# Performance work log

Measured on AMD Instinct MI355X. Metric: run time of the kernel, lower is better.

Reference implementation:

```python
import jax, jax.numpy as jnp
import numpy as np

D_MODEL = 1024
NUM_HEADS = 16
HEAD_DIM = D_MODEL // NUM_HEADS


def setup_inputs() -> dict:
    key = jax.random.key(0)
    ks = jax.random.split(key, 10)
    B, T, D = 2, 2048, D_MODEL
    scale = 1.0 / np.sqrt(D)
    inp = {
        "x": jax.random.normal(ks[0], (B, T, D), dtype=jnp.float32),
        "mask": jax.random.randint(ks[1], (B, T), 0, 2).astype(jnp.int32),
        "Wq": jax.random.normal(ks[2], (D, D), dtype=jnp.float32) * scale,
        "bq": jnp.zeros((D,), dtype=jnp.float32),
        "Wk": jax.random.normal(ks[3], (D, D), dtype=jnp.float32) * scale,
        "bk": jnp.zeros((D,), dtype=jnp.float32),
        "Wv": jax.random.normal(ks[4], (D, D), dtype=jnp.float32) * scale,
        "bv": jnp.zeros((D,), dtype=jnp.float32),
        "Wo": jax.random.normal(ks[5], (D, D), dtype=jnp.float32) * scale,
        "bo": jnp.zeros((D,), dtype=jnp.float32),
    }
    return inp


def reference(x, mask, Wq, bq, Wk, bk, Wv, bv, Wo, bo):
    B, T, D = x.shape
    H, Hd = NUM_HEADS, HEAD_DIM
    # torch Linear: y = x @ W.T + b
    Q = (x @ Wq.T + bq).reshape(B, T, H, Hd).transpose(0, 2, 1, 3)  # [B,H,T,Hd]
    K = (x @ Wk.T + bk).reshape(B, T, H, Hd).transpose(0, 2, 1, 3)
    V = (x @ Wv.T + bv).reshape(B, T, H, Hd).transpose(0, 2, 1, 3)
    scores = jnp.einsum("bhqd,bhkd->bhqk", Q, K) / jnp.sqrt(jnp.float32(Hd))
    # key padding mask: 1=valid, 0=pad -> -inf on padded keys
    key_pad = (mask == 0)[:, None, None, :]  # [B,1,1,T]
    scores = jnp.where(key_pad, -jnp.inf, scores)
    attn = jax.nn.softmax(scores, axis=-1)  # [B,H,T,T]
    # dropout p=0.0 (inference): identity
    context = jnp.einsum("bhqk,bhkd->bhqd", attn, V)  # [B,H,T,Hd]
    context = context.transpose(0, 2, 1, 3).reshape(B, T, D)
    output = context @ Wo.T + bo
    return (output, attn)
```

## Files before the change

kernel.cpp:

```cpp
#include <hip/hip_runtime.h>
#include <math.h>

#define SEQ   2048
#define BATCH 2
#define DM    1024
#define NH    16
#define HD    64
#define MTOT  (BATCH*SEQ)
#define NQSZ  ((size_t)BATCH*NH*SEQ*HD)

typedef __bf16 bf16_t;
typedef __bf16 bf16x4 __attribute__((ext_vector_type(4)));
typedef __bf16 bf16x8 __attribute__((ext_vector_type(8)));
typedef float  f32x4  __attribute__((ext_vector_type(4)));

typedef __attribute__((address_space(1))) void glob_void;
typedef __attribute__((address_space(3))) void lds_void;
#define GL2LDS(gp, lp) __builtin_amdgcn_global_load_lds( \
    (glob_void*)(gp), (lds_void*)(lp), 16, 0, 0)

__global__ __launch_bounds__(256)
void cvt_bf16(const float* __restrict__ in, bf16_t* __restrict__ out, int n)
{
    int i = (blockIdx.x * 256 + threadIdx.x) * 4;
    if (i >= n) return;
    float4 f = *(const float4*)(in + i);
    bf16x4 h;
    h.x = (__bf16)f.x; h.y = (__bf16)f.y; h.z = (__bf16)f.z; h.w = (__bf16)f.w;
    *(bf16x4*)(out + i) = h;
}

template<int MODE>
__global__ __launch_bounds__(256)
void gemm_bt(const bf16_t* __restrict__ A, const bf16_t* __restrict__ W,
             const float* __restrict__ b0p, const float* __restrict__ b1p,
             const float* __restrict__ b2p, void* __restrict__ outp)
{
    __shared__ __align__(16) bf16_t As[128 * 32];
    __shared__ __align__(16) bf16_t Bs[128 * 32];
    const int n0 = blockIdx.x * 128, m0 = blockIdx.y * 128;
    const int tid = threadIdx.x, lane = tid & 63, wave = tid >> 6;
    const int wm = (wave >> 1) * 64, wn = (wave & 1) * 64;
    const int srow = wave * 32 + (lane >> 2);
    const int scol = (lane & 3) * 8;
    const int fr = lane & 15, fk = (lane >> 4) * 8;
    const bf16_t* gA = &A[(size_t)(m0 + srow) * DM + scol];
    const bf16_t* gB = &W[(size_t)(n0 + srow) * DM + scol];
    bf16_t* lA = &As[wave * 1024];
    bf16_t* lB = &Bs[wave * 1024];
    f32x4 acc[4][4] = {};
    for (int k0 = 0; k0 < DM; k0 += 32) {
        GL2LDS(gA,            lA);
        GL2LDS(gA + 16 * DM,  lA + 16 * 32);
        GL2LDS(gB,            lB);
        GL2LDS(gB + 16 * DM,  lB + 16 * 32);
        gA += 32; gB += 32;
        __syncthreads();
        bf16x8 af[4], bv[4];
        #pragma unroll
        for (int mi = 0; mi < 4; ++mi)
            af[mi] = *(const bf16x8*)&As[(wm + mi * 16 + fr) * 32 + fk];
        #pragma unroll
        for (int ni = 0; ni < 4; ++ni)
            bv[ni] = *(const bf16x8*)&Bs[(wn + ni * 16 + fr) * 32 + fk];
        #pragma unroll
        for (int mi = 0; mi < 4; ++mi)
            #pragma unroll
            for (int ni = 0; ni < 4; ++ni)
                acc[mi][ni] = __builtin_amdgcn_mfma_f32_16x16x32_bf16(af[mi], bv[ni], acc[mi][ni], 0, 0, 0);
        __syncthreads();
    }
    const int cr = (lane >> 4) * 4, cc = lane & 15;
    #pragma unroll
    for (int mi = 0; mi < 4; ++mi) {
        #pragma unroll
        for (int ni = 0; ni < 4; ++ni) {
            const int n = n0 + wn + ni * 16 + cc;
            float bn;
            if (MODE == 0) {
                const int which = n >> 10, nn = n & 1023;
                const float* bp = which == 0 ? b0p : (which == 1 ? b1p : b2p);
                bn = bp[nn];
            } else {
                bn = b0p[n];
            }
            #pragma unroll
            for (int v = 0; v < 4; ++v) {
                const int m = m0 + wm + mi * 16 + cr + v;
                const float val = acc[mi][ni][v] + bn;
                if (MODE == 0) {
                    const int which = n >> 10, nn = n & 1023;
                    const int b_ = m >> 11, t = m & (SEQ - 1);
                    const int h = nn >> 6, hd = nn & 63;
                    ((bf16_t*)outp)[(size_t)which * NQSZ +
                        (((size_t)(b_ * NH + h)) * SEQ + t) * HD + hd] = (__bf16)val;
                } else {
                    ((float*)outp)[(size_t)m * DM + n] = val;
                }
            }
        }
    }
}

__global__ __launch_bounds__(256)
void transpose_v(const bf16_t* __restrict__ Vb, bf16_t* __restrict__ Vt)
{
    const int bh = blockIdx.y, t0 = blockIdx.x * 64;
    __shared__ bf16_t L[64][72];
    const bf16_t* src = Vb + (size_t)bh * SEQ * HD;
    bf16_t* dst = Vt + (size_t)bh * HD * SEQ;
    for (int i = threadIdx.x; i < 64 * 64; i += 256) {
        int r = i >> 6, c = i & 63;
        L[c][r] = src[(size_t)(t0 + r) * HD + c];
    }
    __syncthreads();
    for (int i = threadIdx.x; i < 64 * 64; i += 256) {
        int hd = i >> 6, c = i & 63;
        dst[(size_t)hd * SEQ + t0 + c] = L[hd][c];
    }
}

__global__ __launch_bounds__(256, 2)
void fused_attn(const bf16_t* __restrict__ Q, const bf16_t* __restrict__ K,
                const bf16_t* __restrict__ Vt, const int* __restrict__ mask,
                float* __restrict__ attn, bf16_t* __restrict__ ctxb)
{
    __shared__ __align__(16) bf16_t Qs[2 * 128 * 32];
    __shared__ __align__(16) bf16_t Ks[2 * 128 * 32];
    __shared__ __align__(16) bf16_t Vs[4 * 64 * 32];
    __shared__ __align__(16) bf16_t Ps[4][4 * 32 * 32];

    const int bid = blockIdx.x;
    const int grp = bid & 7, g2 = bid >> 3;
    const int bh = grp * 4 + (g2 >> 4);
    const int qt = g2 & 15;
    const int b = bh >> 4, h = bh & 15;
    const int q0 = qt * 128;

    const bf16_t* Qb  = Q  + (size_t)bh * SEQ * HD;
    const bf16_t* Kb  = K  + (size_t)bh * SEQ * HD;
    const bf16_t* Vtb = Vt + (size_t)bh * HD * SEQ;
    const int*    mb  = mask + b * SEQ;
    float*        Ab  = attn + (size_t)bh * SEQ * SEQ;

    const int tid = threadIdx.x, lane = tid & 63, wave = tid >> 6;
    const int wm = wave * 32;
    const int fr = lane & 15, fg = lane >> 4, fk = fg * 8;
    const int cr = fg * 4, cc = fr;
    const int rsw = ((fr >> 2) & 3) << 3;
    const int wsw = fg << 3;

    {
        const int r = tid >> 2, kq = (tid & 3) * 16;
        #pragma unroll
        for (int rr = 0; rr < 2; ++rr)
            #pragma unroll
            for (int j = 0; j < 2; ++j) {
                const int k = kq + j * 8;
                *(uint4*)&Qs[(k >> 5) * 4096 + (r + rr * 64) * 32 + (k & 31)] =
                    *(const uint4*)&Qb[(size_t)(q0 + r + rr * 64) * HD + k];
            }
    }
    __syncthreads();
    bf16x8 qf[2][2];
    #pragma unroll
    for (int mi = 0; mi < 2; ++mi)
        #pragma unroll
        for (int c = 0; c < 2; ++c)
            qf[mi][c] = *(const bf16x8*)&Qs[c * 4096 + (wm + mi * 16 + fr) * 32 + fk];

    float rm[2][4], rl[2][4];
    #pragma unroll
    for (int mi = 0; mi < 2; ++mi)
        #pragma unroll
        for (int v = 0; v < 4; ++v) { rm[mi][v] = -1e30f; rl[mi][v] = 0.f; }

    for (int kt0 = 0; kt0 < SEQ; kt0 += 128) {
        __syncthreads();
        {
            const int r = tid >> 2, kq = (tid & 3) * 16;
            #pragma unroll
            for (int rr = 0; rr < 2; ++rr)
                #pragma unroll
                for (int j = 0; j < 2; ++j) {
                    const int k = kq + j * 8;
                    *(uint4*)&Ks[(k >> 5) * 4096 + (r + rr * 64) * 32 + (k & 31)] =
                        *(const uint4*)&Kb[(size_t)(kt0 + r + rr * 64) * HD + k];
                }
        }
        __syncthreads();
        float ma[8];
        #pragma unroll
        for (int ni = 0; ni < 8; ++ni)
            ma[ni] = mb[kt0 + ni * 16 + cc] ? 0.f : -1e30f;
        f32x4 acc[2][8] = {};
        #pragma unroll
        for (int ni = 0; ni < 8; ++ni) {
            bf16x8 b0 = *(const bf16x8*)&Ks[(ni * 16 + fr) * 32 + fk];
            bf16x8 b1 = *(const bf16x8*)&Ks[4096 + (ni * 16 + fr) * 32 + fk];
            acc[0][ni] = __builtin_amdgcn_mfma_f32_16x16x32_bf16(qf[0][0], b0, acc[0][ni], 0, 0, 0);
            acc[1][ni] = __builtin_amdgcn_mfma_f32_16x16x32_bf16(qf[1][0], b0, acc[1][ni], 0, 0, 0);
            acc[0][ni] = __builtin_amdgcn_mfma_f32_16x16x32_bf16(qf[0][1], b1, acc[0][ni], 0, 0, 0);
            acc[1][ni] = __builtin_amdgcn_mfma_f32_16x16x32_bf16(qf[1][1], b1, acc[1][ni], 0, 0, 0);
        }
        #pragma unroll
        for (int mi = 0; mi < 2; ++mi) {
            #pragma unroll
            for (int v = 0; v < 4; ++v) {
                float tm = -1e30f;
                #pragma unroll
                for (int ni = 0; ni < 8; ++ni) {
                    float s = acc[mi][ni][v] * 0.125f + ma[ni];
                    acc[mi][ni][v] = s;
                    tm = fmaxf(tm, s);
                }
                tm = fmaxf(tm, __shfl_xor(tm, 1));
                tm = fmaxf(tm, __shfl_xor(tm, 2));
                tm = fmaxf(tm, __shfl_xor(tm, 4));
                tm = fmaxf(tm, __shfl_xor(tm, 8));
                const float mn = fmaxf(rm[mi][v], tm);
                float ls = 0.f;
                #pragma unroll
                for (int ni = 0; ni < 8; ++ni)
                    ls += __expf(acc[mi][ni][v] - mn);
                ls += __shfl_xor(ls, 1);
                ls += __shfl_xor(ls, 2);
                ls += __shfl_xor(ls, 4);
                ls += __shfl_xor(ls, 8);
                rl[mi][v] = rl[mi][v] * __expf(rm[mi][v] - mn) + ls;
                rm[mi][v] = mn;
            }
        }
    }

    float invl[2][4];
    #pragma unroll
    for (int mi = 0; mi < 2; ++mi)
        #pragma unroll
        for (int v = 0; v < 4; ++v)
            invl[mi][v] = 1.0f / rl[mi][v];

    f32x4 oac[2][4] = {};
    bf16_t* Pw = &Ps[wave][0];
    for (int kt0 = 0; kt0 < SEQ; kt0 += 128) {
        __syncthreads();
        {
            const int r = tid >> 2, kq = (tid & 3) * 16;
            #pragma unroll
            for (int rr = 0; rr < 2; ++rr)
                #pragma unroll
                for (int j = 0; j < 2; ++j) {
                    const int k = kq + j * 8;
                    *(uint4*)&Ks[(k >> 5) * 4096 + (r + rr * 64) * 32 + (k & 31)] =
                        *(const uint4*)&Kb[(size_t)(kt0 + r + rr * 64) * HD + k];
                }
        }
        {
            const int hd = tid >> 2, ks = tid & 3;
            #pragma unroll
            for (int j = 0; j < 4; ++j)
                *(uint4*)&Vs[ks * 2048 + hd * 32 + j * 8] =
                    *(const uint4*)&Vtb[(size_t)hd * SEQ + kt0 + ks * 32 + j * 8];
        }
        __syncthreads();
        float ma[8];
        #pragma unroll
        for (int ni = 0; ni < 8; ++ni)
            ma[ni] = mb[kt0 + ni * 16 + cc] ? 0.f : -1e30f;
        f32x4 acc[2][8] = {};
        #pragma unroll
        for (int ni = 0; ni < 8; ++ni) {
            bf16x8 b0 = *(const bf16x8*)&Ks[(ni * 16 + fr) * 32 + fk];
            bf16x8 b1 = *(const bf16x8*)&Ks[4096 + (ni * 16 + fr) * 32 + fk];
            acc[0][ni] = __builtin_amdgcn_mfma_f32_16x16x32_bf16(qf[0][0], b0, acc[0][ni], 0, 0, 0);
            acc[1][ni] = __builtin_amdgcn_mfma_f32_16x16x32_bf16(qf[1][0], b0, acc[1][ni], 0, 0, 0);
            acc[0][ni] = __builtin_amdgcn_mfma_f32_16x16x32_bf16(qf[0][1], b1, acc[0][ni], 0, 0, 0);
            acc[1][ni] = __builtin_amdgcn_mfma_f32_16x16x32_bf16(qf[1][1], b1, acc[1][ni], 0, 0, 0);
        }
        #pragma unroll
        for (int mi = 0; mi < 2; ++mi) {
            #pragma unroll
            for (int ni = 0; ni < 8; ++ni) {
                const int ks = ni >> 1, k2 = (ni & 1) * 16 + cc;
                #pragma unroll
                for (int v = 0; v < 4; ++v) {
                    const int rowl = mi * 16 + cr + v;
                    float s = acc[mi][ni][v] * 0.125f + ma[ni];
                    float p = __expf(s - rm[mi][v]) * invl[mi][v];
                    Ab[(size_t)(q0 + wm + rowl) * SEQ + kt0 + ni * 16 + cc] = p;
                    Pw[(ks * 1024 + rowl * 32 + k2) ^ wsw] = (__bf16)p;
                }
            }
        }
        #pragma unroll
        for (int ks = 0; ks < 4; ++ks) {
            bf16x8 pf[2];
            #pragma unroll
            for (int mi = 0; mi < 2; ++mi)
                pf[mi] = *(const bf16x8*)&Pw[(ks * 1024 + (mi * 16 + fr) * 32 + fk) ^ rsw];
            #pragma unroll
            for (int ni = 0; ni < 4; ++ni) {
                bf16x8 vf = *(const bf16x8*)&Vs[ks * 2048 + (ni * 16 + fr) * 32 + fk];
                oac[0][ni] = __builtin_amdgcn_mfma_f32_16x16x32_bf16(pf[0], vf, oac[0][ni], 0, 0, 0);
                oac[1][ni] = __builtin_amdgcn_mfma_f32_16x16x32_bf16(pf[1], vf, oac[1][ni], 0, 0, 0);
            }
        }
    }
    #pragma unroll
    for (int mi = 0; mi < 2; ++mi) {
        #pragma unroll
        for (int ni = 0; ni < 4; ++ni) {
            #pragma unroll
            for (int v = 0; v < 4; ++v) {
                const int t = q0 + wm + mi * 16 + cr + v;
                ctxb[((size_t)b * SEQ + t) * DM + h * HD + ni * 16 + cc] = (__bf16)oac[mi][ni][v];
            }
        }
    }
}

extern "C" void kernel_launch(void* const* d_in, const int* in_sizes, int n_in,
                              void* d_out, int out_size, void* d_ws, size_t ws_size,
                              hipStream_t stream)
{
    const float* x   = (const float*)d_in[0];
    const int*  mask = (const int*)d_in[1];
    const float* Wq  = (const float*)d_in[2];
    const float* bq  = (const float*)d_in[3];
    const float* Wk  = (const float*)d_in[4];
    const float* bk  = (const float*)d_in[5];
    const float* Wv  = (const float*)d_in[6];
    const float* bv  = (const float*)d_in[7];
    const float* Wo  = (const float*)d_in[8];
    const float* bo  = (const float*)d_in[9];

    float* out  = (float*)d_out;
    float* attn = out + (size_t)BATCH * SEQ * DM;

    const size_t NX = (size_t)MTOT * DM;
    const size_t NW = (size_t)DM * DM;

    bf16_t* xb   = (bf16_t*)d_ws;
    bf16_t* Wqb  = xb + NX;
    bf16_t* Wkb  = Wqb + NW;
    bf16_t* Wvb  = Wkb + NW;
    bf16_t* Wob  = Wvb + NW;
    bf16_t* Qb   = Wob + NW;
    bf16_t* Kb   = Qb + NQSZ;
    bf16_t* Vb   = Kb + NQSZ;
    bf16_t* Vt   = Vb + NQSZ;
    bf16_t* ctxb = Vt + NQSZ;

    cvt_bf16<<<dim3(NX / 1024), 256, 0, stream>>>(x, xb, (int)NX);
    cvt_bf16<<<dim3(NW / 1024), 256, 0, stream>>>(Wq, Wqb, (int)NW);
    cvt_bf16<<<dim3(NW / 1024), 256, 0, stream>>>(Wk, Wkb, (int)NW);
    cvt_bf16<<<dim3(NW / 1024), 256, 0, stream>>>(Wv, Wvb, (int)NW);
    cvt_bf16<<<dim3(NW / 1024), 256, 0, stream>>>(Wo, Wob, (int)NW);

    gemm_bt<0><<<dim3(3 * DM / 128, MTOT / 128), 256, 0, stream>>>(xb, Wqb, bq, bk, bv, Qb);

    transpose_v<<<dim3(SEQ / 64, BATCH * NH), 256, 0, stream>>>(Vb, Vt);

    fused_attn<<<dim3(BATCH * NH * (SEQ / 128)), 256, 0, stream>>>(Qb, Kb, Vt, mask, attn, ctxb);

    gemm_bt<1><<<dim3(DM / 128, MTOT / 128), 256, 0, stream>>>(ctxb, Wob, bo, bo, bo, out);
}
```

Before: 782.5 us.

## Fuse V transpose into QKV GEMM, double-buffer K loads, use exp2 softmax

The QKV projection epilogue now writes V directly in transposed layout, which removes the separate transpose kernel. The four weight conversions are merged into one launch. The attention kernel loads Q, K and V tiles asynchronously into LDS with double-buffered K prefetch, and reuses the Q buffer for the P tile. Softmax uses exp2 with the log2e factor folded into the score scale. These changes add barriers and LDS reuse subtleties.

Result: no change. 774.8 us (-1.0%).

```diff
diff --git a/kernel.cpp b/kernel.cpp
--- a/kernel.cpp
+++ b/kernel.cpp
@@ -19,6 +19,8 @@
 #define GL2LDS(gp, lp) __builtin_amdgcn_global_load_lds( \
     (glob_void*)(gp), (lds_void*)(lp), 16, 0, 0)
 
+#define SCL 0.18033688f
+
 __global__ __launch_bounds__(256)
 void cvt_bf16(const float* __restrict__ in, bf16_t* __restrict__ out, int n)
 {
@@ -30,11 +32,27 @@
     *(bf16x4*)(out + i) = h;
 }
 
+__global__ __launch_bounds__(256)
+void cvt_w4(const float* __restrict__ a, const float* __restrict__ b,
+            const float* __restrict__ c, const float* __restrict__ d,
+            bf16_t* __restrict__ out)
+{
+    const int w = blockIdx.y;
+    const float* s;
+    if (w == 0) s = a; else if (w == 1) s = b; else if (w == 2) s = c; else s = d;
+    const int i = (blockIdx.x * 256 + threadIdx.x) * 4;
+    float4 f = *(const float4*)(s + i);
+    bf16x4 h;
+    h.x = (__bf16)f.x; h.y = (__bf16)f.y; h.z = (__bf16)f.z; h.w = (__bf16)f.w;
+    *(bf16x4*)(out + (size_t)w * DM * DM + i) = h;
+}
+
 template<int MODE>
 __global__ __launch_bounds__(256)
 void gemm_bt(const bf16_t* __restrict__ A, const bf16_t* __restrict__ W,
              const float* __restrict__ b0p, const float* __restrict__ b1p,
-             const float* __restrict__ b2p, void* __restrict__ outp)
+             const float* __restrict__ b2p, void* __restrict__ outp,
+             bf16_t* __restrict__ vtp)
 {
     __shared__ __align__(16) bf16_t As[128 * 32];
     __shared__ __align__(16) bf16_t Bs[128 * 32];
@@ -71,6 +89,7 @@
         __syncthreads();
     }
     const int cr = (lane >> 4) * 4, cc = lane & 15;
+    const int which = n0 >> 10;
     #pragma unroll
     for (int mi = 0; mi < 4; ++mi) {
         #pragma unroll
@@ -78,45 +97,39 @@
             const int n = n0 + wn + ni * 16 + cc;
             float bn;
             if (MODE == 0) {
-                const int which = n >> 10, nn = n & 1023;
+                const int nn = n & 1023;
                 const float* bp = which == 0 ? b0p : (which == 1 ? b1p : b2p);
                 bn = bp[nn];
             } else {
                 bn = b0p[n];
             }
-            #pragma unroll
-            for (int v = 0; v < 4; ++v) {
-                const int m = m0 + wm + mi * 16 + cr + v;
-                const float val = acc[mi][ni][v] + bn;
-                if (MODE == 0) {
-                    const int which = n >> 10, nn = n & 1023;
-                    const int b_ = m >> 11, t = m & (SEQ - 1);
-                    const int h = nn >> 6, hd = nn & 63;
-                    ((bf16_t*)outp)[(size_t)which * NQSZ +
-                        (((size_t)(b_ * NH + h)) * SEQ + t) * HD + hd] = (__bf16)val;
-                } else {
-                    ((float*)outp)[(size_t)m * DM + n] = val;
+            if (MODE == 0 && which == 2) {
+                const int m_ = m0 + wm + mi * 16 + cr;
+                const int b_ = m_ >> 11, t0 = m_ & (SEQ - 1);
+                const int nn = n & 1023, h = nn >> 6, hd = nn & 63;
+                bf16x4 pk;
+                pk.x = (__bf16)(acc[mi][ni][0] + bn);
+                pk.y = (__bf16)(acc[mi][ni][1] + bn);
+                pk.z = (__bf16)(acc[mi][ni][2] + bn);
+                pk.w = (__bf16)(acc[mi][ni][3] + bn);
+                *(bf16x4*)&vtp[(((size_t)(b_ * NH + h)) * HD + hd) * SEQ + t0] = pk;
+            } else {
+                #pragma unroll
+                for (int v = 0; v < 4; ++v) {
+                    const int m = m0 + wm + mi * 16 + cr + v;
+                    const float val = acc[mi][ni][v] + bn;
+                    if (MODE == 0) {
+                        const int nn = n & 1023;
+                        const int b_ = m >> 11, t = m & (SEQ - 1);
+                        const int h = nn >> 6, hd = nn & 63;
+                        ((bf16_t*)outp)[(size_t)which * NQSZ +
+                            (((size_t)(b_ * NH + h)) * SEQ + t) * HD + hd] = (__bf16)val;
+                    } else {
+                        ((float*)outp)[(size_t)m * DM + n] = val;
+                    }
                 }
             }
         }
-    }
-}
-
-__global__ __launch_bounds__(256)
-void transpose_v(const bf16_t* __restrict__ Vb, bf16_t* __restrict__ Vt)
-{
-    const int bh = blockIdx.y, t0 = blockIdx.x * 64;
-    __shared__ bf16_t L[64][72];
-    const bf16_t* src = Vb + (size_t)bh * SEQ * HD;
-    bf16_t* dst = Vt + (size_t)bh * HD * SEQ;
-    for (int i = threadIdx.x; i < 64 * 64; i += 256) {
-        int r = i >> 6, c = i & 63;
-        L[c][r] = src[(size_t)(t0 + r) * HD + c];
-    }
-    __syncthreads();
-    for (int i = threadIdx.x; i < 64 * 64; i += 256) {
-        int hd = i >> 6, c = i & 63;
-        dst[(size_t)hd * SEQ + t0 + c] = L[hd][c];
     }
 }
 
@@ -125,10 +138,9 @@
                 const bf16_t* __restrict__ Vt, const int* __restrict__ mask,
                 float* __restrict__ attn, bf16_t* __restrict__ ctxb)
 {
-    __shared__ __align__(16) bf16_t Qs[2 * 128 * 32];
-    __shared__ __align__(16) bf16_t Ks[2 * 128 * 32];
-    __shared__ __align__(16) bf16_t Vs[4 * 64 * 32];
-    __shared__ __align__(16) bf16_t Ps[4][4 * 32 * 32];
+    __shared__ __align__(16) bf16_t PQs[16384];
+    __shared__ __align__(16) bf16_t Ksd[2 * 8192];
+    __shared__ __align__(16) bf16_t Vs[8192];
 
     const int bid = blockIdx.x;
     const int grp = bid & 7, g2 = bid >> 3;
@@ -137,7 +149,7 @@
     const int b = bh >> 4, h = bh & 15;
     const int q0 = qt * 128;
 
-    const bf16_t* Qb  = Q  + (size_t)bh * SEQ * HD;
+    const bf16_t* Qb  = Q  + (size_t)bh * SEQ * HD + (size_t)q0 * HD;
     const bf16_t* Kb  = K  + (size_t)bh * SEQ * HD;
     const bf16_t* Vtb = Vt + (size_t)bh * HD * SEQ;
     const int*    mb  = mask + b * SEQ;
@@ -150,24 +162,28 @@
     const int rsw = ((fr >> 2) & 3) << 3;
     const int wsw = fg << 3;
 
-    {
-        const int r = tid >> 2, kq = (tid & 3) * 16;
-        #pragma unroll
-        for (int rr = 0; rr < 2; ++rr)
-            #pragma unroll
-            for (int j = 0; j < 2; ++j) {
-                const int k = kq + j * 8;
-                *(uint4*)&Qs[(k >> 5) * 4096 + (r + rr * 64) * 32 + (k & 31)] =
-                    *(const uint4*)&Qb[(size_t)(q0 + r + rr * 64) * HD + k];
-            }
-    }
+    int koff[4], voff[4];
+    #pragma unroll
+    for (int i = 0; i < 4; ++i) {
+        const int seg = wave * 4 + i;
+        const int k5 = (lane & 3) * 8;
+        koff[i] = ((seg & 7) * 16 + (lane >> 2)) * HD + (seg >> 3) * 32 + k5;
+        voff[i] = ((seg & 3) * 16 + (lane >> 2)) * SEQ + (seg >> 2) * 32 + k5;
+    }
+    const int segb = wave * 4 * 512;
+
+    #pragma unroll
+    for (int i = 0; i < 4; ++i) GL2LDS(Qb + koff[i], PQs + segb + i * 512);
+    #pragma unroll
+    for (int i = 0; i < 4; ++i) GL2LDS(Kb + koff[i], Ksd + segb + i * 512);
     __syncthreads();
+
     bf16x8 qf[2][2];
     #pragma unroll
     for (int mi = 0; mi < 2; ++mi)
         #pragma unroll
         for (int c = 0; c < 2; ++c)
-            qf[mi][c] = *(const bf16x8*)&Qs[c * 4096 + (wm + mi * 16 + fr) * 32 + fk];
+            qf[mi][c] = *(const bf16x8*)&PQs[c * 4096 + (wm + mi * 16 + fr) * 32 + fk];
 
     float rm[2][4], rl[2][4];
     #pragma unroll
@@ -175,20 +191,16 @@
         #pragma unroll
         for (int v = 0; v < 4; ++v) { rm[mi][v] = -1e30f; rl[mi][v] = 0.f; }
 
-    for (int kt0 = 0; kt0 < SEQ; kt0 += 128) {
-        __syncthreads();
-        {
-            const int r = tid >> 2, kq = (tid & 3) * 16;
-            #pragma unroll
-            for (int rr = 0; rr < 2; ++rr)
-                #pragma unroll
-                for (int j = 0; j < 2; ++j) {
-                    const int k = kq + j * 8;
-                    *(uint4*)&Ks[(k >> 5) * 4096 + (r + rr * 64) * 32 + (k & 31)] =
-                        *(const uint4*)&Kb[(size_t)(kt0 + r + rr * 64) * HD + k];
-                }
-        }
-        __syncthreads();
+    int cur = 0;
+    for (int t = 0; t < 16; ++t) {
+        const int kt0 = t * 128;
+        if (t < 15) {
+            const bf16_t* ns = Kb + (size_t)(kt0 + 128) * HD;
+            bf16_t* nd = Ksd + (cur ^ 1) * 8192 + segb;
+            #pragma unroll
+            for (int i = 0; i < 4; ++i) GL2LDS(ns + koff[i], nd + i * 512);
+        }
+        const bf16_t* Kc = Ksd + cur * 8192;
         float ma[8];
         #pragma unroll
         for (int ni = 0; ni < 8; ++ni)
@@ -196,8 +208,8 @@
         f32x4 acc[2][8] = {};
         #pragma unroll
         for (int ni = 0; ni < 8; ++ni) {
-            bf16x8 b0 = *(const bf16x8*)&Ks[(ni * 16 + fr) * 32 + fk];
-            bf16x8 b1 = *(const bf16x8*)&Ks[4096 + (ni * 16 + fr) * 32 + fk];
+            bf16x8 b0 = *(const bf16x8*)&Kc[(ni * 16 + fr) * 32 + fk];
+            bf16x8 b1 = *(const bf16x8*)&Kc[4096 + (ni * 16 + fr) * 32 + fk];
             acc[0][ni] = __builtin_amdgcn_mfma_f32_16x16x32_bf16(qf[0][0], b0, acc[0][ni], 0, 0, 0);
             acc[1][ni] = __builtin_amdgcn_mfma_f32_16x16x32_bf16(qf[1][0], b0, acc[1][ni], 0, 0, 0);
             acc[0][ni] = __builtin_amdgcn_mfma_f32_16x16x32_bf16(qf[0][1], b1, acc[0][ni], 0, 0, 0);
@@ -210,7 +222,7 @@
                 float tm = -1e30f;
                 #pragma unroll
                 for (int ni = 0; ni < 8; ++ni) {
-                    float s = acc[mi][ni][v] * 0.125f + ma[ni];
+                    float s = acc[mi][ni][v] * SCL + ma[ni];
                     acc[mi][ni][v] = s;
                     tm = fmaxf(tm, s);
                 }
@@ -222,15 +234,17 @@
                 float ls = 0.f;
                 #pragma unroll
                 for (int ni = 0; ni < 8; ++ni)
-                    ls += __expf(acc[mi][ni][v] - mn);
+                    ls += exp2f(acc[mi][ni][v] - mn);
                 ls += __shfl_xor(ls, 1);
                 ls += __shfl_xor(ls, 2);
                 ls += __shfl_xor(ls, 4);
                 ls += __shfl_xor(ls, 8);
-                rl[mi][v] = rl[mi][v] * __expf(rm[mi][v] - mn) + ls;
+                rl[mi][v] = rl[mi][v] * exp2f(rm[mi][v] - mn) + ls;
                 rm[mi][v] = mn;
             }
         }
+        __syncthreads();
+        cur ^= 1;
     }
 
     float invl[2][4];
@@ -241,28 +255,25 @@
             invl[mi][v] = 1.0f / rl[mi][v];
 
     f32x4 oac[2][4] = {};
-    bf16_t* Pw = &Ps[wave][0];
-    for (int kt0 = 0; kt0 < SEQ; kt0 += 128) {
-        __syncthreads();
+    bf16_t* Pw = &PQs[wave * 4096];
+    cur = 0;
+    #pragma unroll
+    for (int i = 0; i < 4; ++i) GL2LDS(Kb + koff[i], Ksd + segb + i * 512);
+    __syncthreads();
+    for (int t = 0; t < 16; ++t) {
+        const int kt0 = t * 128;
+        if (t < 15) {
+            const bf16_t* ns = Kb + (size_t)(kt0 + 128) * HD;
+            bf16_t* nd = Ksd + (cur ^ 1) * 8192 + segb;
+            #pragma unroll
+            for (int i = 0; i < 4; ++i) GL2LDS(ns + koff[i], nd + i * 512);
+        }
         {
-            const int r = tid >> 2, kq = (tid & 3) * 16;
-            #pragma unroll
-            for (int rr = 0; rr < 2; ++rr)
-                #pragma unroll
-                for (int j = 0; j < 2; ++j) {
-                    const int k = kq + j * 8;
-                    *(uint4*)&Ks[(k >> 5) * 4096 + (r + rr * 64) * 32 + (k & 31)] =
-                        *(const uint4*)&Kb[(size_t)(kt0 + r + rr * 64) * HD + k];
-                }
-        }
-        {
-            const int hd = tid >> 2, ks = tid & 3;
-            #pragma unroll
-            for (int j = 0; j < 4; ++j)
-                *(uint4*)&Vs[ks * 2048 + hd * 32 + j * 8] =
-                    *(const uint4*)&Vtb[(size_t)hd * SEQ + kt0 + ks * 32 + j * 8];
-        }
-        __syncthreads();
+            const bf16_t* vsrc = Vtb + kt0;
+            #pragma unroll
+            for (int i = 0; i < 4; ++i) GL2LDS(vsrc + voff[i], Vs + segb + i * 512);
+        }
+        const bf16_t* Kc = Ksd + cur * 8192;
         float ma[8];
         #pragma unroll
         for (int ni = 0; ni < 8; ++ni)
@@ -270,8 +281,8 @@
         f32x4 acc[2][8] = {};
         #pragma unroll
         for (int ni = 0; ni < 8; ++ni) {
-            bf16x8 b0 = *(const bf16x8*)&Ks[(ni * 16 + fr) * 32 + fk];
-            bf16x8 b1 = *(const bf16x8*)&Ks[4096 + (ni * 16 + fr) * 32 + fk];
+            bf16x8 b0 = *(const bf16x8*)&Kc[(ni * 16 + fr) * 32 + fk];
+            bf16x8 b1 = *(const bf16x8*)&Kc[4096 + (ni * 16 + fr) * 32 + fk];
             acc[0][ni] = __builtin_amdgcn_mfma_f32_16x16x32_bf16(qf[0][0], b0, acc[0][ni], 0, 0, 0);
             acc[1][ni] = __builtin_amdgcn_mfma_f32_16x16x32_bf16(qf[1][0], b0, acc[1][ni], 0, 0, 0);
             acc[0][ni] = __builtin_amdgcn_mfma_f32_16x16x32_bf16(qf[0][1], b1, acc[0][ni], 0, 0, 0);
@@ -285,13 +296,14 @@
                 #pragma unroll
                 for (int v = 0; v < 4; ++v) {
                     const int rowl = mi * 16 + cr + v;
-                    float s = acc[mi][ni][v] * 0.125f + ma[ni];
-                    float p = __expf(s - rm[mi][v]) * invl[mi][v];
+                    float s = acc[mi][ni][v] * SCL + ma[ni];
+                    float p = exp2f(s - rm[mi][v]) * invl[mi][v];
                     Ab[(size_t)(q0 + wm + rowl) * SEQ + kt0 + ni * 16 + cc] = p;
                     Pw[(ks * 1024 + rowl * 32 + k2) ^ wsw] = (__bf16)p;
                 }
             }
         }
+        __syncthreads();
         #pragma unroll
         for (int ks = 0; ks < 4; ++ks) {
             bf16x8 pf[2];
@@ -305,6 +317,8 @@
                 oac[1][ni] = __builtin_amdgcn_mfma_f32_16x16x32_bf16(pf[1], vf, oac[1][ni], 0, 0, 0);
             }
         }
+        __syncthreads();
+        cur ^= 1;
     }
     #pragma unroll
     for (int mi = 0; mi < 2; ++mi) {
@@ -342,26 +356,21 @@
 
     bf16_t* xb   = (bf16_t*)d_ws;
     bf16_t* Wqb  = xb + NX;
-    bf16_t* Wkb  = Wqb + NW;
-    bf16_t* Wvb  = Wkb + NW;
-    bf16_t* Wob  = Wvb + NW;
+    bf16_t* Wob  = Wqb + 3 * NW;
     bf16_t* Qb   = Wob + NW;
     bf16_t* Kb   = Qb + NQSZ;
-    bf16_t* Vb   = Kb + NQSZ;
-    bf16_t* Vt   = Vb + NQSZ;
+    bf16_t* Vt   = Kb + NQSZ;
     bf16_t* ctxb = Vt + NQSZ;
 
     cvt_bf16<<<dim3(NX / 1024), 256, 0, stream>>>(x, xb, (int)NX);
-    cvt_bf16<<<dim3(NW / 1024), 256, 0, stream>>>(Wq, Wqb, (int)NW);
-    cvt_bf16<<<dim3(NW / 1024), 256, 0, stream>>>(Wk, Wkb, (int)NW);
-    cvt_bf16<<<dim3(NW / 1024), 256, 0, stream>>>(Wv, Wvb, (int)NW);
-    cvt_bf16<<<dim3(NW / 1024), 256, 0, stream>>>(Wo, Wob, (int)NW);
-
-    gemm_bt<0><<<dim3(3 * DM / 128, MTOT / 128), 256, 0, stream>>>(xb, Wqb, bq, bk, bv, Qb);
-
-    transpose_v<<<dim3(SEQ / 64, BATCH * NH), 256, 0, stream>>>(Vb, Vt);
-
-    fused_attn<<<dim3(BATCH * NH * (SEQ / 128)), 256, 0, stream>>>(Qb, Kb, Vt, mask, attn, ctxb);
-
-    gemm_bt<1><<<dim3(DM / 128, MTOT / 128), 256, 0, stream>>>(ctxb, Wob, bo, bo, bo, out);
-}
+    cvt_w4<<<dim3(NW / 1024, 4), 256, 0, stream>>>(Wq, Wk, Wv, Wo, Wqb);
+
+    gemm_bt<0><<<dim3(3 * DM / 128, MTOT / 128), 256, 0, stream>>>(
+        xb, Wqb, bq, bk, bv, Qb, Vt);
+
+    fused_attn<<<dim3(BATCH * NH * (SEQ / 128)), 256, 0, stream>>>(
+        Qb, Kb, Vt, mask, attn, ctxb);
+
+    gemm_bt<1><<<dim3(DM / 128, MTOT / 128), 256, 0, stream>>>(
+        ctxb, Wob, bo, bo, bo, out, nullptr);
+}
```
